# Kernel optimization log

Hardware: AMD Instinct MI355X
Metric: run time of the kernel (lower is better)

## Reference

```python
import jax, jax.numpy as jnp
import numpy as np

D = 128
EMB = 1024
B, S = 4, 4096


def setup_inputs() -> dict:
    key = jax.random.key(0)
    ks = jax.random.split(key, 7)
    scale = 1.0 / np.sqrt(EMB)
    return {
        "X": jax.random.normal(ks[0], (B, S, EMB), dtype=jnp.float32),
        "lam": jnp.float32(0.8),
        "Wq": jax.random.uniform(ks[1], (EMB, 2 * D), jnp.float32, -scale, scale),
        "bq": jax.random.uniform(ks[2], (2 * D,), jnp.float32, -scale, scale),
        "Wk": jax.random.uniform(ks[3], (EMB, 2 * D), jnp.float32, -scale, scale),
        "bk": jax.random.uniform(ks[4], (2 * D,), jnp.float32, -scale, scale),
        "Wv": jax.random.uniform(ks[5], (EMB, D), jnp.float32, -scale, scale),
        "bv": jax.random.uniform(ks[6], (D,), jnp.float32, -scale, scale),
    }


def reference(X, lam, Wq, bq, Wk, bk, Wv, bv):
    # Projections: Q,K are [B,S,2d]; V is [B,S,d]
    Q = X @ Wq + bq
    K = X @ Wk + bk
    V = X @ Wv + bv
    Q1, Q2 = Q[..., :D], Q[..., D:]
    K1, K2 = K[..., :D], K[..., D:]
    s = 1.0 / jnp.sqrt(jnp.float32(D))
    # Dual QK^T scores [B,S,S]
    A1 = jnp.einsum("bqd,bkd->bqk", Q1, K1) * s
    A2 = jnp.einsum("bqd,bkd->bqk", Q2, K2) * s
    P = jax.nn.softmax(A1, axis=-1) - lam * jax.nn.softmax(A2, axis=-1)
    return jnp.einsum("bqk,bkd->bqd", P, V)
```

## Files before the change

### kernel.cpp

```cpp
#include <hip/hip_runtime.h>
#include <hip/hip_bf16.h>


typedef __attribute__((ext_vector_type(8))) short bf16x8;
typedef __attribute__((ext_vector_type(4))) float f32x4;
typedef __attribute__((ext_vector_type(16))) float f32x16;

#define MFMA16(a, b, c) __builtin_amdgcn_mfma_f32_16x16x32_bf16((a), (b), (c), 0, 0, 0)
#define MFMA32(a, b, c) __builtin_amdgcn_mfma_f32_32x32x16_bf16((a), (b), (c), 0, 0, 0)

typedef const __attribute__((address_space(1))) void gas_void;
typedef __attribute__((address_space(3))) void las_void;
#define GLOAD16(G, L) __builtin_amdgcn_global_load_lds((gas_void*)(G), (las_void*)(L), 16, 0, 0)

__device__ __forceinline__ unsigned short f2bf(float x) {
    union { float f; unsigned u; } v; v.f = x;
    return (unsigned short)((v.u + 0x7FFFu + ((v.u >> 16) & 1u)) >> 16);
}
__device__ __forceinline__ unsigned pk2bf(float a, float b) {
    __hip_bfloat162 h = __float22bfloat162_rn(float2{a, b});
    union { __hip_bfloat162 h2; unsigned u; } cv; cv.h2 = h;
    return cv.u;
}
__device__ __forceinline__ float fexp2(float x) {
    float r; asm("v_exp_f32 %0, %1" : "=v"(r) : "v"(x)); return r;
}

__global__ __launch_bounds__(256) void wtrans_kernel(
    const float* __restrict__ Wq, const float* __restrict__ Wk,
    const float* __restrict__ Wv, unsigned short* __restrict__ Wt) {
    int tid = blockIdx.x * 256 + threadIdx.x;
    int k = tid & 1023, n = tid >> 10;
    float v;
    if (n < 256)      v = Wq[k * 256 + n];
    else if (n < 512) v = Wk[k * 256 + (n - 256)];
    else              v = Wv[k * 128 + (n - 512)];
    Wt[tid] = f2bf(v);
}

__global__ __launch_bounds__(256) void proj_kernel(
    const float* __restrict__ X, const unsigned short* __restrict__ Wt,
    const float* __restrict__ bq, const float* __restrict__ bk,
    const float* __restrict__ bv,
    unsigned short* __restrict__ Qs, unsigned short* __restrict__ Kb,
    unsigned short* __restrict__ Vb) {
    __shared__ alignas(16) char lds[16384];
    const int nt = blockIdx.y;
    const int m0 = blockIdx.x * 128;
    const int t = threadIdx.x, w = t >> 6, l = t & 63, c = l & 15, g = l >> 4;
    const int wm = w >> 1, wn = w & 1;
    const unsigned short* Wrow = Wt + (long)(nt * 128) * 1024;

    f32x4 acc[4][4];
    const f32x4 fz = {0.f, 0.f, 0.f, 0.f};
#pragma unroll
    for (int i = 0; i < 4; i++)
#pragma unroll
        for (int j = 0; j < 4; j++) acc[i][j] = fz;

    const int srow = t >> 1, sh = t & 1;
    const int sswz = (srow & 7) << 4;
    for (int k0 = 0; k0 < 1024; k0 += 32) {
        const float* xs = X + (long)(m0 + srow) * 1024 + k0 + sh * 16;
        float4 f0 = *(const float4*)(xs + 0);
        float4 f1 = *(const float4*)(xs + 4);
        float4 f2 = *(const float4*)(xs + 8);
        float4 f3 = *(const float4*)(xs + 12);
        const unsigned short* wsc = Wrow + (long)srow * 1024 + k0 + sh * 16;
        uint4 w0 = *(const uint4*)(wsc + 0);
        uint4 w1 = *(const uint4*)(wsc + 8);
        uint4 xa, xb;
        xa.x = pk2bf(f0.x, f0.y); xa.y = pk2bf(f0.z, f0.w);
        xa.z = pk2bf(f1.x, f1.y); xa.w = pk2bf(f1.z, f1.w);
        xb.x = pk2bf(f2.x, f2.y); xb.y = pk2bf(f2.z, f2.w);
        xb.z = pk2bf(f3.x, f3.y); xb.w = pk2bf(f3.z, f3.w);
        int base = srow * 64 + sh * 32;
        *(uint4*)(lds + ((base + 0) ^ sswz)) = xa;
        *(uint4*)(lds + ((base + 16) ^ sswz)) = xb;
        *(uint4*)(lds + 8192 + ((base + 0) ^ sswz)) = w0;
        *(uint4*)(lds + 8192 + ((base + 16) ^ sswz)) = w1;
        __syncthreads();

        bf16x8 af[4];
#pragma unroll
        for (int am = 0; am < 4; am++) {
            int r_ = wm * 64 + am * 16 + c;
            af[am] = *(const bf16x8*)(lds + ((r_ * 64 + g * 16) ^ ((c & 7) << 4)));
        }
#pragma unroll
        for (int bn = 0; bn < 4; bn++) {
            int r_ = wn * 64 + bn * 16 + c;
            bf16x8 bfr = *(const bf16x8*)(lds + 8192 + ((r_ * 64 + g * 16) ^ ((c & 7) << 4)));
#pragma unroll
            for (int am = 0; am < 4; am++) acc[am][bn] = MFMA16(af[am], bfr, acc[am][bn]);
        }
        __syncthreads();
    }

    const float QSCALE = 0.08838834764831845f * 1.4426950408889634f;
    const float* bias; float scale; unsigned short* outp; int ostride, ocol0, boff;
    if (nt < 2)      { bias = bq; boff = nt * 128;       scale = QSCALE; outp = Qs; ostride = 256; ocol0 = nt * 128; }
    else if (nt < 4) { bias = bk; boff = (nt - 2) * 128; scale = 1.0f;   outp = Kb; ostride = 256; ocol0 = (nt - 2) * 128; }
    else             { bias = bv; boff = 0;              scale = 1.0f;   outp = Vb; ostride = 128; ocol0 = 0; }
#pragma unroll
    for (int bn = 0; bn < 4; bn++) {
        int ncol = wn * 64 + bn * 16 + c;
        float bb = bias[boff + ncol];
#pragma unroll
        for (int am = 0; am < 4; am++) {
#pragma unroll
            for (int r = 0; r < 4; r++) {
                long row = m0 + wm * 64 + am * 16 + 4 * g + r;
                outp[row * ostride + ocol0 + ncol] = f2bf((acc[am][bn][r] + bb) * scale);
            }
        }
    }
}

__global__ __launch_bounds__(256) void vtrans_kernel(
    const unsigned short* __restrict__ Vb, unsigned short* __restrict__ Vt) {
    __shared__ unsigned short lds[64][72];
    const int bid = blockIdx.x;
    const int db = bid & 1, sb = (bid >> 1) & 63, b = bid >> 7;
    const int s0 = sb * 64, d0 = db * 64;
    const int t = threadIdx.x;
    const int r = t >> 2, c4 = t & 3;
    const unsigned short* src = Vb + ((long)(b * 4096 + s0 + r)) * 128 + d0;
    uint4 u0 = *(const uint4*)(src + c4 * 8);
    uint4 u1 = *(const uint4*)(src + (c4 + 4) * 8);
    *(uint4*)(&lds[r][c4 * 8]) = u0;
    *(uint4*)(&lds[r][(c4 + 4) * 8]) = u1;
    __syncthreads();
    const int dd = t >> 2;
    unsigned short* dst = Vt + ((long)(b * 128 + d0 + dd)) * 4096 + s0;
#pragma unroll
    for (int cc2 = 0; cc2 < 2; cc2++) {
        int cc = c4 + cc2 * 4;
        unsigned short tmp[8];
#pragma unroll
        for (int j = 0; j < 8; j++) tmp[j] = lds[cc * 8 + j][dd];
        *(uint4*)(dst + cc * 8) = *(const uint4*)tmp;
    }
}

__global__ __launch_bounds__(256, 2) void attn3_kernel(
    const unsigned short* __restrict__ Qs, const unsigned short* __restrict__ Kb,
    const unsigned short* __restrict__ Vt,
    float* __restrict__ Po, float* __restrict__ Ps, int nsplit, int ks) {
    __shared__ alignas(16) char lds[65536];
    const int t = threadIdx.x;
    const int w = t >> 6, l = t & 63, r31 = l & 31, hi = l >> 5;

    const int total = gridDim.x;
    const int lin = (blockIdx.x & 7) * (total >> 3) + (blockIdx.x >> 3);
    const int qb = lin & 31;
    const int g2 = lin >> 5;
    const int br = g2 & 1;
    const int sp = g2 >> 1;
    const int split = sp % nsplit, b = sp / nsplit;

    const long qrow = (long)b * 4096 + qb * 128 + w * 32 + r31;
    bf16x8 qf[8];
    const unsigned short* Qp = Qs + qrow * 256 + br * 128 + hi * 8;
#pragma unroll
    for (int ds = 0; ds < 8; ds++) qf[ds] = *(const bf16x8*)(Qp + ds * 16);

    f32x16 o[4];
    const f32x16 oz = {};
#pragma unroll
    for (int dt = 0; dt < 4; dt++) o[dt] = oz;
    float m = -1e30f, s = 0.f;

    const int krowA = t >> 4;
    const int kcolS = (((t & 15) * 16) - krowA * 16) & 255;
    const int vdA = t >> 2;
    const int vcolS = (((t & 3) * 16) - (((vdA >> 1) & 3) * 16)) & 63;
    const long kbb = (long)b * 4096;
    const char* kSrc0 = (const char*)Kb + (kbb + krowA) * 512 + br * 256 + kcolS;
    const char* vSrc0 = (const char*)Vt + ((long)b * 128 + vdA) * 8192 + vcolS;
    char* dst0 = lds + w * 1024;

    const int kb0 = split * ks;
    const int nt = ks >> 6;
#define STAGE(KB_, BUF_)                                                       \
    {                                                                          \
        const char* kp_ = kSrc0 + (long)(KB_)*512;                             \
        const char* vp_ = vSrc0 + (long)(KB_)*2;                               \
        char* d_ = dst0 + (BUF_)*32768;                                        \
        GLOAD16(kp_, d_);                                                      \
        GLOAD16(kp_ + 8192, d_ + 4096);                                        \
        GLOAD16(kp_ + 16384, d_ + 8192);                                       \
        GLOAD16(kp_ + 24576, d_ + 12288);                                      \
        GLOAD16(vp_, d_ + 16384);                                              \
        GLOAD16(vp_ + 524288, d_ + 20480);                                     \
        GLOAD16(vp_ + 64, d_ + 24576);                                         \
        GLOAD16(vp_ + 524288 + 64, d_ + 28672);                                \
    }

    int kro[8];
#pragma unroll
    for (int ds = 0; ds < 8; ds++)
        kro[ds] = r31 * 256 + ((ds * 32 + hi * 16 + r31 * 16) & 255);
    int vro0[4], vro1[4];
#pragma unroll
    for (int dt = 0; dt < 4; dt++) {
        int vr = dt * 32 + r31, rot = ((vr >> 1) & 3) * 16;
        vro0[dt] = 16384 + vr * 64 + ((hi * 16 + rot) & 63);
        vro1[dt] = 16384 + vr * 64 + ((32 + hi * 16 + rot) & 63);
    }

    STAGE(kb0, 0);

    for (int it = 0; it < nt; it++) {
        asm volatile("s_waitcnt vmcnt(0)" ::: "memory");
        __builtin_amdgcn_sched_barrier(0);
        __builtin_amdgcn_s_barrier();
        __builtin_amdgcn_sched_barrier(0);
        if (it + 1 < nt) STAGE(kb0 + ((it + 1) << 6), (it + 1) & 1);
        const char* bufp = lds + (it & 1) * 32768;

        f32x16 pa0 = oz, pb0_ = oz, pa1 = oz, pb1_ = oz;
        __builtin_amdgcn_s_setprio(1);
#pragma unroll
        for (int ds = 0; ds < 4; ds++) {
            bf16x8 k0a = *(const bf16x8*)(bufp + kro[ds]);
            bf16x8 k0b = *(const bf16x8*)(bufp + kro[ds + 4]);
            bf16x8 k1a = *(const bf16x8*)(bufp + 8192 + kro[ds]);
            bf16x8 k1b = *(const bf16x8*)(bufp + 8192 + kro[ds + 4]);
            pa0 = MFMA32(k0a, qf[ds], pa0);
            pb0_ = MFMA32(k0b, qf[ds + 4], pb0_);
            pa1 = MFMA32(k1a, qf[ds], pa1);
            pb1_ = MFMA32(k1b, qf[ds + 4], pb1_);
        }
        __builtin_amdgcn_s_setprio(0);
        f32x16 p0, p1;
#pragma unroll
        for (int i = 0; i < 16; i++) { p0[i] = pa0[i] + pb0_[i]; p1[i] = pa1[i] + pb1_[i]; }

        float x0 = fmaxf(fmaxf(p0[0], p0[1]), fmaxf(p0[2], p0[3]));
        float x1 = fmaxf(fmaxf(p0[4], p0[5]), fmaxf(p0[6], p0[7]));
        float x2 = fmaxf(fmaxf(p0[8], p0[9]), fmaxf(p0[10], p0[11]));
        float x3 = fmaxf(fmaxf(p0[12], p0[13]), fmaxf(p0[14], p0[15]));
        float y0 = fmaxf(fmaxf(p1[0], p1[1]), fmaxf(p1[2], p1[3]));
        float y1 = fmaxf(fmaxf(p1[4], p1[5]), fmaxf(p1[6], p1[7]));
        float y2 = fmaxf(fmaxf(p1[8], p1[9]), fmaxf(p1[10], p1[11]));
        float y3 = fmaxf(fmaxf(p1[12], p1[13]), fmaxf(p1[14], p1[15]));
        float lmx = fmaxf(fmaxf(fmaxf(x0, x1), fmaxf(x2, x3)),
                          fmaxf(fmaxf(y0, y1), fmaxf(y2, y3)));
        lmx = fmaxf(lmx, __shfl_xor(lmx, 32));
        if (__any(lmx > m + 8.f)) {
            float mn = fmaxf(m, lmx);
            float al = fexp2(m - mn);
            s *= al; m = mn;
#pragma unroll
            for (int dt = 0; dt < 4; dt++) o[dt] *= al;
        }
        float pe0[16], pe1[16];
#pragma unroll
        for (int i = 0; i < 16; i++) { pe0[i] = fexp2(p0[i] - m); pe1[i] = fexp2(p1[i] - m); }
        float s0 = ((pe0[0] + pe0[1]) + (pe0[2] + pe0[3])) +
                   ((pe0[4] + pe0[5]) + (pe0[6] + pe0[7]));
        float s1 = ((pe0[8] + pe0[9]) + (pe0[10] + pe0[11])) +
                   ((pe0[12] + pe0[13]) + (pe0[14] + pe0[15]));
        float s2 = ((pe1[0] + pe1[1]) + (pe1[2] + pe1[3])) +
                   ((pe1[4] + pe1[5]) + (pe1[6] + pe1[7]));
        float s3 = ((pe1[8] + pe1[9]) + (pe1[10] + pe1[11])) +
                   ((pe1[12] + pe1[13]) + (pe1[14] + pe1[15]));
        float ps_ = (s0 + s1) + (s2 + s3);
        ps_ += __shfl_xor(ps_, 32);
        s += ps_;

        unsigned cA = pk2bf(pe0[0], pe0[1]), cB = pk2bf(pe0[2], pe0[3]);
        unsigned cC = pk2bf(pe0[4], pe0[5]), cD = pk2bf(pe0[6], pe0[7]);
        asm volatile("v_permlane32_swap_b32 %0, %1" : "+v"(cA), "+v"(cC));
        asm volatile("v_permlane32_swap_b32 %0, %1" : "+v"(cB), "+v"(cD));
        unsigned dA = pk2bf(pe0[8], pe0[9]), dB = pk2bf(pe0[10], pe0[11]);
        unsigned dC = pk2bf(pe0[12], pe0[13]), dD = pk2bf(pe0[14], pe0[15]);
        asm volatile("v_permlane32_swap_b32 %0, %1" : "+v"(dA), "+v"(dC));
        asm volatile("v_permlane32_swap_b32 %0, %1" : "+v"(dB), "+v"(dD));
        unsigned eA = pk2bf(pe1[0], pe1[1]), eB = pk2bf(pe1[2], pe1[3]);
        unsigned eC = pk2bf(pe1[4], pe1[5]), eD = pk2bf(pe1[6], pe1[7]);
        asm volatile("v_permlane32_swap_b32 %0, %1" : "+v"(eA), "+v"(eC));
        asm volatile("v_permlane32_swap_b32 %0, %1" : "+v"(eB), "+v"(eD));
        unsigned fA = pk2bf(pe1[8], pe1[9]), fB = pk2bf(pe1[10], pe1[11]);
        unsigned fC = pk2bf(pe1[12], pe1[13]), fD = pk2bf(pe1[14], pe1[15]);
        asm volatile("v_permlane32_swap_b32 %0, %1" : "+v"(fA), "+v"(fC));
        asm volatile("v_permlane32_swap_b32 %0, %1" : "+v"(fB), "+v"(fD));
        union { uint4 u; bf16x8 v; } q00, q01, q10, q11;
        q00.u = uint4{cA, cB, cC, cD};
        q01.u = uint4{dA, dB, dC, dD};
        q10.u = uint4{eA, eB, eC, eD};
        q11.u = uint4{fA, fB, fC, fD};

        __builtin_amdgcn_s_setprio(1);
#pragma unroll
        for (int dt = 0; dt < 4; dt++) {
            bf16x8 v00 = *(const bf16x8*)(bufp + vro0[dt]);
            bf16x8 v01 = *(const bf16x8*)(bufp + vro1[dt]);
            bf16x8 v10 = *(const bf16x8*)(bufp + 8192 + vro0[dt]);
            bf16x8 v11 = *(const bf16x8*)(bufp + 8192 + vro1[dt]);
            o[dt] = MFMA32(v00, q00.v, o[dt]);
            o[dt] = MFMA32(v01, q01.v, o[dt]);
            o[dt] = MFMA32(v10, q10.v, o[dt]);
            o[dt] = MFMA32(v11, q11.v, o[dt]);
        }
        __builtin_amdgcn_s_setprio(0);
    }

    float* po = Po + ((qrow * nsplit + split) * 2 + br) * 128;
#pragma unroll
    for (int dt = 0; dt < 4; dt++) {
#pragma unroll
        for (int rg = 0; rg < 4; rg++) {
            float4 v;
            v.x = o[dt][rg * 4 + 0];
            v.y = o[dt][rg * 4 + 1];
            v.z = o[dt][rg * 4 + 2];
            v.w = o[dt][rg * 4 + 3];
            *(float4*)(po + dt * 32 + rg * 8 + hi * 4) = v;
        }
    }
    if (hi == 0)
        *(float2*)(Ps + (qrow * nsplit + split) * 4 + br * 2) = float2{m, s};
#undef STAGE
}

__global__ __launch_bounds__(256) void combine_kernel(
    const float* __restrict__ Po, const float* __restrict__ Ps,
    const float* __restrict__ lam_p, float* __restrict__ out, int nsplit) {
    int tid = blockIdx.x * 256 + threadIdx.x;
    int q = tid >> 5, dq = (tid & 31) * 4;
    float M1 = -1e30f, M2 = -1e30f;
    for (int s = 0; s < nsplit; s++) {
        float4 st = *(const float4*)(Ps + (long)(q * nsplit + s) * 4);
        M1 = fmaxf(M1, st.x); M2 = fmaxf(M2, st.z);
    }
    float S1 = 0.f, S2 = 0.f;
    float a0 = 0.f, a1 = 0.f, a2 = 0.f, a3 = 0.f;
    float b0 = 0.f, b1 = 0.f, b2 = 0.f, b3 = 0.f;
    for (int s = 0; s < nsplit; s++) {
        float4 st = *(const float4*)(Ps + (long)(q * nsplit + s) * 4);
        float w1 = fexp2(st.x - M1), w2 = fexp2(st.z - M2);
        S1 += st.y * w1; S2 += st.w * w2;
        const float* p1 = Po + (((long)q * nsplit + s) * 2 + 0) * 128 + dq;
        const float* p2 = Po + (((long)q * nsplit + s) * 2 + 1) * 128 + dq;
        float4 v1 = *(const float4*)p1;
        float4 v2 = *(const float4*)p2;
        a0 += v1.x * w1; a1 += v1.y * w1; a2 += v1.z * w1; a3 += v1.w * w1;
        b0 += v2.x * w2; b1 += v2.y * w2; b2 += v2.z * w2; b3 += v2.w * w2;
    }
    float lam = *lam_p;
    float i1 = 1.f / S1, i2 = lam / S2;
    float4 v;
    v.x = a0 * i1 - b0 * i2;
    v.y = a1 * i1 - b1 * i2;
    v.z = a2 * i1 - b2 * i2;
    v.w = a3 * i1 - b3 * i2;
    *(float4*)(out + (long)q * 128 + dq) = v;
}

extern "C" void kernel_launch(void* const* d_in, const int* in_sizes, int n_in,
                              void* d_out, int out_size, void* d_ws, size_t ws_size,
                              hipStream_t stream) {
    const float* X   = (const float*)d_in[0];
    const float* lam = (const float*)d_in[1];
    const float* Wq  = (const float*)d_in[2];
    const float* bq  = (const float*)d_in[3];
    const float* Wk  = (const float*)d_in[4];
    const float* bk  = (const float*)d_in[5];
    const float* Wv  = (const float*)d_in[6];
    const float* bv  = (const float*)d_in[7];
    char* ws = (char*)d_ws;
    unsigned short* Qs = (unsigned short*)(ws);
    unsigned short* Kb = (unsigned short*)(ws + (8u << 20));
    unsigned short* Vb = (unsigned short*)(ws + (16u << 20));
    unsigned short* Vt = (unsigned short*)(ws + (20u << 20));
    unsigned short* Wt = (unsigned short*)(ws + (24u << 20));
    const size_t base = (size_t)26 << 20;
    const size_t NQ = 16384;
    int nsplit = 1;
    if (ws_size >= base + NQ * 4 * 2 * 128 * 4 + NQ * 4 * 4 * 4)      nsplit = 4;
    else if (ws_size >= base + NQ * 2 * 2 * 128 * 4 + NQ * 2 * 4 * 4) nsplit = 2;
    float* Po = (float*)(ws + base);
    float* Ps = (float*)(ws + base + NQ * (size_t)nsplit * 2 * 128 * 4);

    wtrans_kernel<<<2560, 256, 0, stream>>>(Wq, Wk, Wv, Wt);
    proj_kernel<<<dim3(128, 5), 256, 0, stream>>>(X, Wt, bq, bk, bv, Qs, Kb, Vb);
    vtrans_kernel<<<512, 256, 0, stream>>>(Vb, Vt);
    attn3_kernel<<<256 * nsplit, 256, 0, stream>>>(Qs, Kb, Vt, Po, Ps,
                                                   nsplit, 4096 / nsplit);
    combine_kernel<<<2048, 256, 0, stream>>>(Po, Ps, lam, (float*)d_out, nsplit);
}
```

Baseline: 157.4 us.

## Double-buffer projection GEMM with async LDS loads and 32x32 MFMA tiles

```diff
diff --git a/kernel.cpp b/kernel.cpp
--- a/kernel.cpp
+++ b/kernel.cpp
@@ -44,58 +44,97 @@
     const float* __restrict__ bv,
     unsigned short* __restrict__ Qs, unsigned short* __restrict__ Kb,
     unsigned short* __restrict__ Vb) {
-    __shared__ alignas(16) char lds[16384];
+    __shared__ alignas(16) char lds[65536];
     const int nt = blockIdx.y;
     const int m0 = blockIdx.x * 128;
-    const int t = threadIdx.x, w = t >> 6, l = t & 63, c = l & 15, g = l >> 4;
+    const int t = threadIdx.x, w = t >> 6, r31 = (t & 63) & 31, hi = (t & 63) >> 5;
     const int wm = w >> 1, wn = w & 1;
-    const unsigned short* Wrow = Wt + (long)(nt * 128) * 1024;
-
-    f32x4 acc[4][4];
-    const f32x4 fz = {0.f, 0.f, 0.f, 0.f};
-#pragma unroll
-    for (int i = 0; i < 4; i++)
-#pragma unroll
-        for (int j = 0; j < 4; j++) acc[i][j] = fz;
-
-    const int srow = t >> 1, sh = t & 1;
-    const int sswz = (srow & 7) << 4;
-    for (int k0 = 0; k0 < 1024; k0 += 32) {
-        const float* xs = X + (long)(m0 + srow) * 1024 + k0 + sh * 16;
-        float4 f0 = *(const float4*)(xs + 0);
-        float4 f1 = *(const float4*)(xs + 4);
-        float4 f2 = *(const float4*)(xs + 8);
-        float4 f3 = *(const float4*)(xs + 12);
-        const unsigned short* wsc = Wrow + (long)srow * 1024 + k0 + sh * 16;
-        uint4 w0 = *(const uint4*)(wsc + 0);
-        uint4 w1 = *(const uint4*)(wsc + 8);
-        uint4 xa, xb;
-        xa.x = pk2bf(f0.x, f0.y); xa.y = pk2bf(f0.z, f0.w);
-        xa.z = pk2bf(f1.x, f1.y); xa.w = pk2bf(f1.z, f1.w);
-        xb.x = pk2bf(f2.x, f2.y); xb.y = pk2bf(f2.z, f2.w);
-        xb.z = pk2bf(f3.x, f3.y); xb.w = pk2bf(f3.z, f3.w);
-        int base = srow * 64 + sh * 32;
-        *(uint4*)(lds + ((base + 0) ^ sswz)) = xa;
-        *(uint4*)(lds + ((base + 16) ^ sswz)) = xb;
-        *(uint4*)(lds + 8192 + ((base + 0) ^ sswz)) = w0;
-        *(uint4*)(lds + 8192 + ((base + 16) ^ sswz)) = w1;
-        __syncthreads();
-
-        bf16x8 af[4];
-#pragma unroll
-        for (int am = 0; am < 4; am++) {
-            int r_ = wm * 64 + am * 16 + c;
-            af[am] = *(const bf16x8*)(lds + ((r_ * 64 + g * 16) ^ ((c & 7) << 4)));
-        }
-#pragma unroll
-        for (int bn = 0; bn < 4; bn++) {
-            int r_ = wn * 64 + bn * 16 + c;
-            bf16x8 bfr = *(const bf16x8*)(lds + 8192 + ((r_ * 64 + g * 16) ^ ((c & 7) << 4)));
-#pragma unroll
-            for (int am = 0; am < 4; am++) acc[am][bn] = MFMA16(af[am], bfr, acc[am][bn]);
-        }
-        __syncthreads();
-    }
+
+    const int rowB = t >> 3;
+    const int bcolS = (((t & 7) * 16) - (rowB & 7) * 16) & 127;
+    const char* bSrc0 = (const char*)Wt + (long)(nt * 128 + rowB) * 2048 + bcolS;
+    char* dst0 = lds + w * 1024;
+#define PSTAGE_B(ST_, BUF_)                                                    \
+    {                                                                          \
+        const char* b_ = bSrc0 + (long)(ST_)*128;                              \
+        char* d_ = dst0 + (BUF_)*32768 + 16384;                                \
+        GLOAD16(b_, d_);                                                       \
+        GLOAD16(b_ + 65536, d_ + 4096);                                        \
+        GLOAD16(b_ + 131072, d_ + 8192);                                       \
+        GLOAD16(b_ + 196608, d_ + 12288);                                      \
+    }
+    const int arow = t >> 1, ah = t & 1;
+    const float* aSrc = X + (long)(m0 + arow) * 1024 + ah * 32;
+    const int arot = (arow & 7) * 16;
+#define ASTAGE(ST_, BUF_)                                                      \
+    {                                                                          \
+        const float* xs = aSrc + (ST_)*64;                                     \
+        float4 f0 = *(const float4*)(xs + 0);                                  \
+        float4 f1 = *(const float4*)(xs + 4);                                  \
+        float4 f2 = *(const float4*)(xs + 8);                                  \
+        float4 f3 = *(const float4*)(xs + 12);                                 \
+        float4 f4 = *(const float4*)(xs + 16);                                 \
+        float4 f5 = *(const float4*)(xs + 20);                                 \
+        float4 f6 = *(const float4*)(xs + 24);                                 \
+        float4 f7 = *(const float4*)(xs + 28);                                 \
+        uint4 u0, u1, u2, u3;                                                  \
+        u0.x = pk2bf(f0.x, f0.y); u0.y = pk2bf(f0.z, f0.w);                    \
+        u0.z = pk2bf(f1.x, f1.y); u0.w = pk2bf(f1.z, f1.w);                    \
+        u1.x = pk2bf(f2.x, f2.y); u1.y = pk2bf(f2.z, f2.w);                    \
+        u1.z = pk2bf(f3.x, f3.y); u1.w = pk2bf(f3.z, f3.w);                    \
+        u2.x = pk2bf(f4.x, f4.y); u2.y = pk2bf(f4.z, f4.w);                    \
+        u2.z = pk2bf(f5.x, f5.y); u2.w = pk2bf(f5.z, f5.w);                    \
+        u3.x = pk2bf(f6.x, f6.y); u3.y = pk2bf(f6.z, f6.w);                    \
+        u3.z = pk2bf(f7.x, f7.y); u3.w = pk2bf(f7.z, f7.w);                    \
+        char* d_ = lds + (BUF_)*32768 + arow * 128;                            \
+        *(uint4*)(d_ + ((ah * 64 + 0 + arot) & 127)) = u0;                     \
+        *(uint4*)(d_ + ((ah * 64 + 16 + arot) & 127)) = u1;                    \
+        *(uint4*)(d_ + ((ah * 64 + 32 + arot) & 127)) = u2;                    \
+        *(uint4*)(d_ + ((ah * 64 + 48 + arot) & 127)) = u3;                    \
+    }
+
+    int aro[2][4], bro[2][4];
+#pragma unroll
+    for (int mi = 0; mi < 2; mi++)
+#pragma unroll
+        for (int ks = 0; ks < 4; ks++) {
+            int rot = (ks * 32 + hi * 16 + (r31 & 7) * 16) & 127;
+            aro[mi][ks] = (wm * 64 + mi * 32 + r31) * 128 + rot;
+            bro[mi][ks] = 16384 + (wn * 64 + mi * 32 + r31) * 128 + rot;
+        }
+
+    f32x16 acc[2][2];
+    const f32x16 oz = {};
+    acc[0][0] = oz; acc[0][1] = oz; acc[1][0] = oz; acc[1][1] = oz;
+
+    PSTAGE_B(0, 0);
+    ASTAGE(0, 0);
+    for (int st = 0; st < 16; st++) {
+        asm volatile("s_waitcnt vmcnt(0) lgkmcnt(0)" ::: "memory");
+        __builtin_amdgcn_sched_barrier(0);
+        __builtin_amdgcn_s_barrier();
+        __builtin_amdgcn_sched_barrier(0);
+        if (st + 1 < 16) {
+            PSTAGE_B(st + 1, (st + 1) & 1);
+            ASTAGE(st + 1, (st + 1) & 1);
+        }
+        const char* bp = lds + (st & 1) * 32768;
+        __builtin_amdgcn_s_setprio(1);
+#pragma unroll
+        for (int ks = 0; ks < 4; ks++) {
+            bf16x8 a0 = *(const bf16x8*)(bp + aro[0][ks]);
+            bf16x8 a1 = *(const bf16x8*)(bp + aro[1][ks]);
+            bf16x8 b0 = *(const bf16x8*)(bp + bro[0][ks]);
+            bf16x8 b1 = *(const bf16x8*)(bp + bro[1][ks]);
+            acc[0][0] = MFMA32(a0, b0, acc[0][0]);
+            acc[0][1] = MFMA32(a0, b1, acc[0][1]);
+            acc[1][0] = MFMA32(a1, b0, acc[1][0]);
+            acc[1][1] = MFMA32(a1, b1, acc[1][1]);
+        }
+        __builtin_amdgcn_s_setprio(0);
+    }
+#undef PSTAGE_B
+#undef ASTAGE
 
     const float QSCALE = 0.08838834764831845f * 1.4426950408889634f;
     const float* bias; float scale; unsigned short* outp; int ostride, ocol0, boff;
@@ -103,15 +142,17 @@
     else if (nt < 4) { bias = bk; boff = (nt - 2) * 128; scale = 1.0f;   outp = Kb; ostride = 256; ocol0 = (nt - 2) * 128; }
     else             { bias = bv; boff = 0;              scale = 1.0f;   outp = Vb; ostride = 128; ocol0 = 0; }
 #pragma unroll
-    for (int bn = 0; bn < 4; bn++) {
-        int ncol = wn * 64 + bn * 16 + c;
+    for (int ni = 0; ni < 2; ni++) {
+        int ncol = wn * 64 + ni * 32 + r31;
         float bb = bias[boff + ncol];
 #pragma unroll
-        for (int am = 0; am < 4; am++) {
-#pragma unroll
-            for (int r = 0; r < 4; r++) {
-                long row = m0 + wm * 64 + am * 16 + 4 * g + r;
-                outp[row * ostride + ocol0 + ncol] = f2bf((acc[am][bn][r] + bb) * scale);
+        for (int mi = 0; mi < 2; mi++) {
+#pragma unroll
+            for (int reg = 0; reg < 16; reg++) {
+                int mrow = wm * 64 + mi * 32 + (reg & 3) + 8 * (reg >> 2) + 4 * hi;
+                long row = m0 + mrow;
+                outp[row * ostride + ocol0 + ncol] =
+                    f2bf((acc[mi][ni][reg] + bb) * scale);
             }
         }
     }
```

After: 182.2 us. 15.8% more time.
